# Kernel optimization log

Hardware: AMD Instinct MI355X
Metric: run time of the kernel (lower is better)

Reference implementation:

```python
import jax, jax.numpy as jnp
import numpy as np

H = 32  # hidden size


def _lstm_layer(x_sbi, w_ih, w_hh, b_ih, b_hh):
    # x_sbi: [S, B, in]; w_ih: [4H, in]; w_hh: [4H, H] (torch gate order i,f,g,o)
    S, B, _ = x_sbi.shape
    # precompute input projections for all timesteps: [S, B, 4H]
    xg = jnp.einsum('sbi,gi->sbg', x_sbi, w_ih) + (b_ih + b_hh)

    def step(carry, xg_t):
        h, c = carry
        gates = xg_t + h @ w_hh.T  # [B, 4H]
        i, f, g, o = jnp.split(gates, 4, axis=-1)
        i = jax.nn.sigmoid(i)
        f = jax.nn.sigmoid(f)
        g = jnp.tanh(g)
        o = jax.nn.sigmoid(o)
        c = f * c + i * g
        h = o * jnp.tanh(c)
        return (h, c), h

    h0 = jnp.zeros((B, H), x_sbi.dtype)
    c0 = jnp.zeros((B, H), x_sbi.dtype)
    (h_last, _), hs = jax.lax.scan(step, (h0, c0), xg)
    return hs, h_last  # hs: [S, B, H]


def setup_inputs() -> dict:
    key = jax.random.key(0)
    ks = jax.random.split(key, 12)
    B, S = 4096, 512
    s = 1.0 / np.sqrt(H)  # torch default uniform(-1/sqrt(H), 1/sqrt(H))
    u = lambda k, shape: jax.random.uniform(k, shape, jnp.float32, -s, s)
    return {
        'x': jax.random.normal(ks[0], (B, S, 1), jnp.float32),
        'w_ih0': u(ks[1], (4 * H, 1)),
        'w_hh0': u(ks[2], (4 * H, H)),
        'b_ih0': u(ks[3], (4 * H,)),
        'b_hh0': u(ks[4], (4 * H,)),
        'w_ih1': u(ks[5], (4 * H, H)),
        'w_hh1': u(ks[6], (4 * H, H)),
        'b_ih1': u(ks[7], (4 * H,)),
        'b_hh1': u(ks[8], (4 * H,)),
        'fc1_w': u(ks[9], (16, H)),
        'fc1_b': u(ks[9], (16,)),
        'fc2_w': u(ks[10], (1, 16)),
        'fc2_b': u(ks[11], (1,)),
    }


def reference(x, w_ih0, w_hh0, b_ih0, b_hh0, w_ih1, w_hh1, b_ih1, b_hh1,
              fc1_w, fc1_b, fc2_w, fc2_b):
    x_sbi = jnp.swapaxes(x, 0, 1)  # [S, B, 1]
    hs1, _ = _lstm_layer(x_sbi, w_ih0, w_hh0, b_ih0, b_hh0)
    _, h_last = _lstm_layer(hs1, w_ih1, w_hh1, b_ih1, b_hh1)  # last timestep of layer 2
    y = h_last @ fc1_w.T + fc1_b
    y = jnp.where(y >= 0, y, 0.2 * y)  # leaky_relu(0.2)
    y = y @ fc2_w.T + fc2_b
    return y  # [B, 1]
```

## Files before the change

kernel.cpp:

```cpp
#include <hip/hip_runtime.h>

#define H 32
#define SEQ 512
#define BM 16
#define NTHREADS 512
#define HSTRIDE 40

typedef _Float16 half8 __attribute__((ext_vector_type(8)));
typedef _Float16 f16x2 __attribute__((ext_vector_type(2)));
typedef __attribute__((ext_vector_type(4))) float f32x4;
typedef __attribute__((ext_vector_type(2))) float f32x2;

#define L2E 1.44269504088896340736f

__device__ __forceinline__ float rcp_(float x)  { return __builtin_amdgcn_rcpf(x); }
__device__ __forceinline__ float exp2_(float x) { return __builtin_amdgcn_exp2f(x); }
#define MFMA16(A, B, C) __builtin_amdgcn_mfma_f32_16x16x32_f16((A), (B), (C), 0, 0, 0)

__device__ __forceinline__ f32x2 cell2(const f32x4& ga, const f32x4& gb, f32x2& cst) {
    f32x2 ei = {exp2_(ga[0]), exp2_(gb[0])};
    f32x2 ef = {exp2_(ga[1]), exp2_(gb[1])};
    f32x2 eg = {exp2_(ga[2]), exp2_(gb[2])};
    f32x2 eo = {exp2_(ga[3]), exp2_(gb[3])};
    f32x2 A  = 1.f + ei, F = 1.f + ef;
    f32x2 Gp = eg + 1.f, Gm = eg - 1.f;
    f32x2 t1 = A * Gp;
    f32x2 num = __builtin_elementwise_fma(cst, t1, Gm * F);
    f32x2 den = F * t1;
    f32x2 r1 = {rcp_(den.x), rcp_(den.y)};
    f32x2 cn = num * r1;
    cst = cn;
    f32x2 arg = __builtin_elementwise_min(cn * (2.f * L2E), (f32x2)80.f);
    f32x2 ec = {exp2_(arg.x), exp2_(arg.y)};
    f32x2 dh = (1.f + eo) * (ec + 1.f);
    f32x2 r2 = {rcp_(dh.x), rcp_(dh.y)};
    return (ec - 1.f) * r2;
}

__global__ __launch_bounds__(NTHREADS, 2) void lstm_kernel(
    const float* __restrict__ x,
    const float* __restrict__ w_ih0,
    const float* __restrict__ w_hh0,
    const float* __restrict__ b_ih0, const float* __restrict__ b_hh0,
    const float* __restrict__ w_ih1,
    const float* __restrict__ w_hh1,
    const float* __restrict__ b_ih1, const float* __restrict__ b_hh1,
    const float* __restrict__ fc1_w,
    const float* __restrict__ fc1_b,
    const float* __restrict__ fc2_w,
    const float* __restrict__ fc2_b,
    float* __restrict__ out)
{
    __shared__ __align__(16) float    xbufT[(SEQ + 1) * BM];
    __shared__ __align__(16) _Float16 h1s[4][BM * HSTRIDE];
    __shared__ __align__(16) _Float16 h2s[2][BM * HSTRIDE];
    __shared__ __align__(16) float    h2f[BM * 33];
    __shared__ __align__(16) float    yb[BM * 17];

    const int tid  = threadIdx.x;
    const int lane = tid & 63;
    const int wv   = tid >> 6;
    const int role = wv >> 2;
    const int w    = wv & 3;
    const int c    = lane & 15;
    const int q    = lane >> 4;
    const int r0   = blockIdx.x * BM;

    {
        const int row = tid >> 5;
        const int s0  = (tid & 31) * 16;
        const float* xr = x + (size_t)(r0 + row) * SEQ + s0;
        #pragma unroll
        for (int i = 0; i < 16; i += 4) {
            float4 v = *(const float4*)&xr[i];
            xbufT[(s0 + i + 0) * BM + row] = v.x;
            xbufT[(s0 + i + 1) * BM + row] = v.y;
            xbufT[(s0 + i + 2) * BM + row] = v.z;
            xbufT[(s0 + i + 3) * BM + row] = v.w;
        }
    }
    for (int i = tid; i < 4 * BM * HSTRIDE; i += NTHREADS) ((_Float16*)h1s)[i] = (_Float16)0.f;
    for (int i = tid; i < 2 * BM * HSTRIDE; i += NTHREADS) ((_Float16*)h2s)[i] = (_Float16)0.f;

    const float gsc[4] = { -L2E, -L2E, 2.f * L2E, -L2E };
    const float wsc = gsc[c & 3];
    const int kb = 8 * q;
    const int m = c;

    half8 wA[2], wB[2];
    f32x4 biasv[2], wxv[2];
    #pragma unroll
    for (int k = 0; k < 2; ++k) {
        const int u     = 8 * w + 2 * q + k;
        const int worig = (c & 3) * H + 8 * w + 2 * (c >> 2) + k;
        if (role == 0) {
            const float* p = &w_hh0[worig * H + kb];
            #pragma unroll
            for (int j = 0; j < 8; ++j) wA[k][j] = (_Float16)(p[j] * wsc);
            #pragma unroll
            for (int g = 0; g < 4; ++g) {
                biasv[k][g] = (b_ih0[g * H + u] + b_hh0[g * H + u]) * gsc[g];
                wxv[k][g]   = w_ih0[g * H + u] * gsc[g];
            }
        } else {
            const float* p = &w_ih1[worig * H + kb];
            #pragma unroll
            for (int j = 0; j < 8; ++j) wA[k][j] = (_Float16)(p[j] * wsc);
            p = &w_hh1[worig * H + kb];
            #pragma unroll
            for (int j = 0; j < 8; ++j) wB[k][j] = (_Float16)(p[j] * wsc);
            #pragma unroll
            for (int g = 0; g < 4; ++g)
                biasv[k][g] = (b_ih1[g * H + u] + b_hh1[g * H + u]) * gsc[g];
        }
    }

    f32x2 cst = {0.f, 0.f};
    f32x2 hl  = {0.f, 0.f};

    const int fofs  = c * HSTRIDE + kb;
    const int whofs = m * HSTRIDE + 8 * w + 2 * q;

    f32x4 P[2][2] = {};

    __syncthreads();

    if (role == 0) __builtin_amdgcn_s_setprio(1);

    float xv = xbufT[m];

    for (int tb = 0; tb < 516; tb += 4) {
        #pragma unroll
        for (int p = 0; p < 4; ++p) {
            const int t = tb + p;
            if (role == 0) {
                if (t < 512) {
                    f32x4 pre[2];
                    #pragma unroll
                    for (int k = 0; k < 2; ++k) {
                        #pragma unroll
                        for (int j = 0; j < 4; ++j) pre[k][j] = fmaf(xv, wxv[k][j], biasv[k][j]);
                    }
                    half8 a1 = *(const half8*)(&h1s[(p + 3) & 3][0] + fofs);
                    f32x4 g0 = MFMA16(wA[0], a1, pre[0]);
                    f32x4 g1 = MFMA16(wA[1], a1, pre[1]);
                    f32x2 hv = cell2(g0, g1, cst);
                    f16x2 hp; hp[0] = (_Float16)hv.x; hp[1] = (_Float16)hv.y;
                    *(f16x2*)(&h1s[p][0] + whofs) = hp;
                    xv = xbufT[(t + 1) * BM + m];
                }
            } else {
                if (t >= 2 && t < 514) {
                    half8 a2 = *(const half8*)(&h2s[(p + 1) & 1][0] + fofs);
                    f32x4 g0 = MFMA16(wB[0], a2, P[p & 1][0]);
                    f32x4 g1 = MFMA16(wB[1], a2, P[p & 1][1]);
                    f32x2 hv = cell2(g0, g1, cst);
                    hl = hv;
                    f16x2 hp; hp[0] = (_Float16)hv.x; hp[1] = (_Float16)hv.y;
                    *(f16x2*)(&h2s[p & 1][0] + whofs) = hp;
                }
                if (t >= 1 && t < 513) {
                    half8 a1n = *(const half8*)(&h1s[(p + 3) & 3][0] + fofs);
                    P[(p + 1) & 1][0] = MFMA16(wA[0], a1n, biasv[0]);
                    P[(p + 1) & 1][1] = MFMA16(wA[1], a1n, biasv[1]);
                }
            }
            __syncthreads();
        }
    }

    if (role == 0) __builtin_amdgcn_s_setprio(0);

    if (role == 1) {
        h2f[m * 33 + (8 * w + 2 * q + 0)] = hl.x;
        h2f[m * 33 + (8 * w + 2 * q + 1)] = hl.y;
    }
    __syncthreads();
    if (tid < BM * 16) {
        int rr = tid >> 4, j = tid & 15;
        float acc = fc1_b[j];
        #pragma unroll
        for (int k = 0; k < H; ++k) acc += fc1_w[j * H + k] * h2f[rr * 33 + k];
        acc = acc >= 0.f ? acc : 0.2f * acc;
        yb[rr * 17 + j] = acc * fc2_w[j];
    }
    __syncthreads();
    if (tid < BM) {
        float acc = fc2_b[0];
        #pragma unroll
        for (int j = 0; j < 16; ++j) acc += yb[tid * 17 + j];
        out[r0 + tid] = acc;
    }
}

extern "C" void kernel_launch(void* const* d_in, const int* in_sizes, int n_in,
                              void* d_out, int out_size, void* d_ws, size_t ws_size,
                              hipStream_t stream) {
    const float* x     = (const float*)d_in[0];
    const float* w_ih0 = (const float*)d_in[1];
    const float* w_hh0 = (const float*)d_in[2];
    const float* b_ih0 = (const float*)d_in[3];
    const float* b_hh0 = (const float*)d_in[4];
    const float* w_ih1 = (const float*)d_in[5];
    const float* w_hh1 = (const float*)d_in[6];
    const float* b_ih1 = (const float*)d_in[7];
    const float* b_hh1 = (const float*)d_in[8];
    const float* fc1_w = (const float*)d_in[9];
    const float* fc1_b = (const float*)d_in[10];
    const float* fc2_w = (const float*)d_in[11];
    const float* fc2_b = (const float*)d_in[12];
    float* out = (float*)d_out;

    const int B = in_sizes[0] / SEQ;
    hipLaunchKernelGGL(lstm_kernel, dim3(B / BM), dim3(NTHREADS), 0, stream,
                       x, w_ih0, w_hh0, b_ih0, b_hh0, w_ih1, w_hh1, b_ih1, b_hh1,
                       fc1_w, fc1_b, fc2_w, fc2_b, out);
}
```

Baseline: 253.6 us.

## Halve batch tile to 8 rows with 4 waves, doubling MFMAs per wave

Shrinks each block from 16 batch rows and 8 waves to 8 rows and 4 waves. Each wave now covers 16 hidden units and issues four MFMAs per step, selecting results by lane half. This doubles the grid size and shrinks the barrier group, meant to improve CU fill and cut per-step sync latency. In exchange, half of the MFMA columns are duplicated work. It also adds an s_sleep stagger on the upper half of blocks.

New measurement: 275.4 us. +8.6%, slower.

```diff
diff --git a/kernel.cpp b/kernel.cpp
--- a/kernel.cpp
+++ b/kernel.cpp
@@ -2,8 +2,8 @@
 
 #define H 32
 #define SEQ 512
-#define BM 16
-#define NTHREADS 512
+#define BM 8
+#define NTHREADS 256
 #define HSTRIDE 40
 
 typedef _Float16 half8 __attribute__((ext_vector_type(8)));
@@ -60,23 +60,26 @@
     const int tid  = threadIdx.x;
     const int lane = tid & 63;
     const int wv   = tid >> 6;
-    const int role = wv >> 2;
-    const int w    = wv & 3;
+    const int role = wv >> 1;
+    const int wh   = wv & 1;
     const int c    = lane & 15;
     const int q    = lane >> 4;
+    const int row  = c & 7;
+    const int ch   = c >> 3;
+    const int U0   = 16 * wh;
     const int r0   = blockIdx.x * BM;
 
     {
-        const int row = tid >> 5;
-        const int s0  = (tid & 31) * 16;
-        const float* xr = x + (size_t)(r0 + row) * SEQ + s0;
+        const int xrow = tid >> 5;
+        const int s0   = (tid & 31) * 16;
+        const float* xr = x + (size_t)(r0 + xrow) * SEQ + s0;
         #pragma unroll
         for (int i = 0; i < 16; i += 4) {
             float4 v = *(const float4*)&xr[i];
-            xbufT[(s0 + i + 0) * BM + row] = v.x;
-            xbufT[(s0 + i + 1) * BM + row] = v.y;
-            xbufT[(s0 + i + 2) * BM + row] = v.z;
-            xbufT[(s0 + i + 3) * BM + row] = v.w;
+            xbufT[(s0 + i + 0) * BM + xrow] = v.x;
+            xbufT[(s0 + i + 1) * BM + xrow] = v.y;
+            xbufT[(s0 + i + 2) * BM + xrow] = v.z;
+            xbufT[(s0 + i + 3) * BM + xrow] = v.w;
         }
     }
     for (int i = tid; i < 4 * BM * HSTRIDE; i += NTHREADS) ((_Float16*)h1s)[i] = (_Float16)0.f;
@@ -85,49 +88,54 @@
     const float gsc[4] = { -L2E, -L2E, 2.f * L2E, -L2E };
     const float wsc = gsc[c & 3];
     const int kb = 8 * q;
-    const int m = c;
-
-    half8 wA[2], wB[2];
+
+    half8 wA[4], wB[4];
     f32x4 biasv[2], wxv[2];
     #pragma unroll
-    for (int k = 0; k < 2; ++k) {
-        const int u     = 8 * w + 2 * q + k;
-        const int worig = (c & 3) * H + 8 * w + 2 * (c >> 2) + k;
+    for (int kk = 0; kk < 4; ++kk) {
+        const int worig = (c & 3) * H + U0 + 8 * (kk >> 1) + 2 * (c >> 2) + (kk & 1);
         if (role == 0) {
             const float* p = &w_hh0[worig * H + kb];
             #pragma unroll
-            for (int j = 0; j < 8; ++j) wA[k][j] = (_Float16)(p[j] * wsc);
-            #pragma unroll
-            for (int g = 0; g < 4; ++g) {
-                biasv[k][g] = (b_ih0[g * H + u] + b_hh0[g * H + u]) * gsc[g];
-                wxv[k][g]   = w_ih0[g * H + u] * gsc[g];
-            }
+            for (int j = 0; j < 8; ++j) wA[kk][j] = (_Float16)(p[j] * wsc);
         } else {
             const float* p = &w_ih1[worig * H + kb];
             #pragma unroll
-            for (int j = 0; j < 8; ++j) wA[k][j] = (_Float16)(p[j] * wsc);
+            for (int j = 0; j < 8; ++j) wA[kk][j] = (_Float16)(p[j] * wsc);
             p = &w_hh1[worig * H + kb];
             #pragma unroll
-            for (int j = 0; j < 8; ++j) wB[k][j] = (_Float16)(p[j] * wsc);
-            #pragma unroll
-            for (int g = 0; g < 4; ++g)
+            for (int j = 0; j < 8; ++j) wB[kk][j] = (_Float16)(p[j] * wsc);
+        }
+    }
+    #pragma unroll
+    for (int k = 0; k < 2; ++k) {
+        const int u = U0 + 8 * ch + 2 * q + k;
+        #pragma unroll
+        for (int g = 0; g < 4; ++g) {
+            if (role == 0) {
+                biasv[k][g] = (b_ih0[g * H + u] + b_hh0[g * H + u]) * gsc[g];
+                wxv[k][g]   = w_ih0[g * H + u] * gsc[g];
+            } else {
                 biasv[k][g] = (b_ih1[g * H + u] + b_hh1[g * H + u]) * gsc[g];
+            }
         }
     }
 
     f32x2 cst = {0.f, 0.f};
     f32x2 hl  = {0.f, 0.f};
 
-    const int fofs  = c * HSTRIDE + kb;
-    const int whofs = m * HSTRIDE + 8 * w + 2 * q;
-
-    f32x4 P[2][2] = {};
+    const int fofs  = row * HSTRIDE + kb;
+    const int whofs = row * HSTRIDE + U0 + 8 * ch + 2 * q;
+
+    f32x4 P[2][4] = {};
 
     __syncthreads();
 
+    if (blockIdx.x & 256) __builtin_amdgcn_s_sleep(7);
+
     if (role == 0) __builtin_amdgcn_s_setprio(1);
 
-    float xv = xbufT[m];
+    float xv = xbufT[row];
 
     for (int tb = 0; tb < 516; tb += 4) {
         #pragma unroll
@@ -135,25 +143,37 @@
             const int t = tb + p;
             if (role == 0) {
                 if (t < 512) {
-                    f32x4 pre[2];
+                    f32x4 pre0, pre1;
                     #pragma unroll
-                    for (int k = 0; k < 2; ++k) {
-                        #pragma unroll
-                        for (int j = 0; j < 4; ++j) pre[k][j] = fmaf(xv, wxv[k][j], biasv[k][j]);
+                    for (int j = 0; j < 4; ++j) {
+                        pre0[j] = fmaf(xv, wxv[0][j], biasv[0][j]);
+                        pre1[j] = fmaf(xv, wxv[1][j], biasv[1][j]);
                     }
                     half8 a1 = *(const half8*)(&h1s[(p + 3) & 3][0] + fofs);
-                    f32x4 g0 = MFMA16(wA[0], a1, pre[0]);
-                    f32x4 g1 = MFMA16(wA[1], a1, pre[1]);
+                    f32x4 d0 = MFMA16(wA[0], a1, pre0);
+                    f32x4 d1 = MFMA16(wA[1], a1, pre1);
+                    f32x4 d2 = MFMA16(wA[2], a1, pre0);
+                    f32x4 d3 = MFMA16(wA[3], a1, pre1);
+                    f32x4 g0, g1;
+                    #pragma unroll
+                    for (int j = 0; j < 4; ++j) { g0[j] = ch ? d2[j] : d0[j];
+                                                  g1[j] = ch ? d3[j] : d1[j]; }
                     f32x2 hv = cell2(g0, g1, cst);
                     f16x2 hp; hp[0] = (_Float16)hv.x; hp[1] = (_Float16)hv.y;
                     *(f16x2*)(&h1s[p][0] + whofs) = hp;
-                    xv = xbufT[(t + 1) * BM + m];
+                    xv = xbufT[(t + 1) * BM + row];
                 }
             } else {
                 if (t >= 2 && t < 514) {
                     half8 a2 = *(const half8*)(&h2s[(p + 1) & 1][0] + fofs);
-                    f32x4 g0 = MFMA16(wB[0], a2, P[p & 1][0]);
-                    f32x4 g1 = MFMA16(wB[1], a2, P[p & 1][1]);
+                    f32x4 d0 = MFMA16(wB[0], a2, P[p & 1][0]);
+                    f32x4 d1 = MFMA16(wB[1], a2, P[p & 1][1]);
+                    f32x4 d2 = MFMA16(wB[2], a2, P[p & 1][2]);
+                    f32x4 d3 = MFMA16(wB[3], a2, P[p & 1][3]);
+                    f32x4 g0, g1;
+                    #pragma unroll
+                    for (int j = 0; j < 4; ++j) { g0[j] = ch ? d2[j] : d0[j];
+                                                  g1[j] = ch ? d3[j] : d1[j]; }
                     f32x2 hv = cell2(g0, g1, cst);
                     hl = hv;
                     f16x2 hp; hp[0] = (_Float16)hv.x; hp[1] = (_Float16)hv.y;
@@ -163,6 +183,8 @@
                     half8 a1n = *(const half8*)(&h1s[(p + 3) & 3][0] + fofs);
                     P[(p + 1) & 1][0] = MFMA16(wA[0], a1n, biasv[0]);
                     P[(p + 1) & 1][1] = MFMA16(wA[1], a1n, biasv[1]);
+                    P[(p + 1) & 1][2] = MFMA16(wA[2], a1n, biasv[0]);
+                    P[(p + 1) & 1][3] = MFMA16(wA[3], a1n, biasv[1]);
                 }
             }
             __syncthreads();
@@ -172,8 +194,8 @@
     if (role == 0) __builtin_amdgcn_s_setprio(0);
 
     if (role == 1) {
-        h2f[m * 33 + (8 * w + 2 * q + 0)] = hl.x;
-        h2f[m * 33 + (8 * w + 2 * q + 1)] = hl.y;
+        h2f[row * 33 + (U0 + 8 * ch + 2 * q + 0)] = hl.x;
+        h2f[row * 33 + (U0 + 8 * ch + 2 * q + 1)] = hl.y;
     }
     __syncthreads();
     if (tid < BM * 16) {
```

## Make each wave own four batch rows for both layers and drop block barriers

Applied to the files above, without the earlier changes.

Work is split by batch row instead of by layer. Each 64-lane wave computes layer 1, layer 2 and the layer-2 input projection for its own four rows across all 32 hidden units. Because each wave only reads hidden state it wrote itself, the per-timestep __syncthreads is removed and the block shrinks to 256 threads. In exchange each wave issues 8 MFMAs per matrix product and keeps only a quarter of the outputs, selected per lane, which raises MFMA work about fourfold. Each wave also holds all three weight matrices in registers, and layer-1 and layer-2 cells now run serially in one wave rather than on separate waves.

Measured after the change: 383.9 us. 1.51x slower.

```diff
diff --git a/kernel.cpp b/kernel.cpp
--- a/kernel.cpp
+++ b/kernel.cpp
@@ -3,7 +3,7 @@
 #define H 32
 #define SEQ 512
 #define BM 16
-#define NTHREADS 512
+#define NTHREADS 256
 #define HSTRIDE 40
 
 typedef _Float16 half8 __attribute__((ext_vector_type(8)));
@@ -37,7 +37,20 @@
     return (ec - 1.f) * r2;
 }
 
-__global__ __launch_bounds__(NTHREADS, 2) void lstm_kernel(
+__device__ __forceinline__ f32x4 sel4(const f32x4& a0, const f32x4& a1,
+                                      const f32x4& a2, const f32x4& a3,
+                                      bool s0, bool s1) {
+    f32x4 r;
+    #pragma unroll
+    for (int j = 0; j < 4; ++j) {
+        float t0 = s0 ? a1[j] : a0[j];
+        float t1 = s0 ? a3[j] : a2[j];
+        r[j] = s1 ? t1 : t0;
+    }
+    return r;
+}
+
+__global__ __launch_bounds__(NTHREADS, 1) void lstm_kernel(
     const float* __restrict__ x,
     const float* __restrict__ w_ih0,
     const float* __restrict__ w_hh0,
@@ -52,7 +65,7 @@
     float* __restrict__ out)
 {
     __shared__ __align__(16) float    xbufT[(SEQ + 1) * BM];
-    __shared__ __align__(16) _Float16 h1s[4][BM * HSTRIDE];
+    __shared__ __align__(16) _Float16 h1s[2][BM * HSTRIDE];
     __shared__ __align__(16) _Float16 h2s[2][BM * HSTRIDE];
     __shared__ __align__(16) float    h2f[BM * 33];
     __shared__ __align__(16) float    yb[BM * 17];
@@ -60,123 +73,123 @@
     const int tid  = threadIdx.x;
     const int lane = tid & 63;
     const int wv   = tid >> 6;
-    const int role = wv >> 2;
-    const int w    = wv & 3;
     const int c    = lane & 15;
     const int q    = lane >> 4;
+    const int s    = c >> 2;
+    const bool sb0 = s & 1, sb1 = (s >> 1) & 1;
+    const int row  = 4 * wv + (c & 3);
     const int r0   = blockIdx.x * BM;
 
     {
-        const int row = tid >> 5;
-        const int s0  = (tid & 31) * 16;
-        const float* xr = x + (size_t)(r0 + row) * SEQ + s0;
-        #pragma unroll
-        for (int i = 0; i < 16; i += 4) {
+        const int xrow = tid >> 4;
+        const int s0_  = (tid & 15) * 32;
+        const float* xr = x + (size_t)(r0 + xrow) * SEQ + s0_;
+        #pragma unroll
+        for (int i = 0; i < 32; i += 4) {
             float4 v = *(const float4*)&xr[i];
-            xbufT[(s0 + i + 0) * BM + row] = v.x;
-            xbufT[(s0 + i + 1) * BM + row] = v.y;
-            xbufT[(s0 + i + 2) * BM + row] = v.z;
-            xbufT[(s0 + i + 3) * BM + row] = v.w;
-        }
-    }
-    for (int i = tid; i < 4 * BM * HSTRIDE; i += NTHREADS) ((_Float16*)h1s)[i] = (_Float16)0.f;
-    for (int i = tid; i < 2 * BM * HSTRIDE; i += NTHREADS) ((_Float16*)h2s)[i] = (_Float16)0.f;
+            xbufT[(s0_ + i + 0) * BM + xrow] = v.x;
+            xbufT[(s0_ + i + 1) * BM + xrow] = v.y;
+            xbufT[(s0_ + i + 2) * BM + xrow] = v.z;
+            xbufT[(s0_ + i + 3) * BM + xrow] = v.w;
+        }
+    }
+    for (int i = tid; i < 2 * BM * HSTRIDE; i += NTHREADS) {
+        ((_Float16*)h1s)[i] = (_Float16)0.f;
+        ((_Float16*)h2s)[i] = (_Float16)0.f;
+    }
 
     const float gsc[4] = { -L2E, -L2E, 2.f * L2E, -L2E };
     const float wsc = gsc[c & 3];
     const int kb = 8 * q;
-    const int m = c;
-
-    half8 wA[2], wB[2];
-    f32x4 biasv[2], wxv[2];
+
+    half8 wA0[8], wI1[8], wH1[8];
+    #pragma unroll
+    for (int kk = 0; kk < 8; ++kk) {
+        const int worig = (c & 3) * H + 8 * (kk >> 1) + 2 * (c >> 2) + (kk & 1);
+        const float* p = &w_hh0[worig * H + kb];
+        #pragma unroll
+        for (int j = 0; j < 8; ++j) wA0[kk][j] = (_Float16)(p[j] * wsc);
+        p = &w_ih1[worig * H + kb];
+        #pragma unroll
+        for (int j = 0; j < 8; ++j) wI1[kk][j] = (_Float16)(p[j] * wsc);
+        p = &w_hh1[worig * H + kb];
+        #pragma unroll
+        for (int j = 0; j < 8; ++j) wH1[kk][j] = (_Float16)(p[j] * wsc);
+    }
+    f32x4 b1v[2], wxv[2], b2v[2];
     #pragma unroll
     for (int k = 0; k < 2; ++k) {
-        const int u     = 8 * w + 2 * q + k;
-        const int worig = (c & 3) * H + 8 * w + 2 * (c >> 2) + k;
-        if (role == 0) {
-            const float* p = &w_hh0[worig * H + kb];
-            #pragma unroll
-            for (int j = 0; j < 8; ++j) wA[k][j] = (_Float16)(p[j] * wsc);
-            #pragma unroll
-            for (int g = 0; g < 4; ++g) {
-                biasv[k][g] = (b_ih0[g * H + u] + b_hh0[g * H + u]) * gsc[g];
-                wxv[k][g]   = w_ih0[g * H + u] * gsc[g];
+        const int u = 8 * s + 2 * q + k;
+        #pragma unroll
+        for (int g = 0; g < 4; ++g) {
+            b1v[k][g] = (b_ih0[g * H + u] + b_hh0[g * H + u]) * gsc[g];
+            wxv[k][g] = w_ih0[g * H + u] * gsc[g];
+            b2v[k][g] = (b_ih1[g * H + u] + b_hh1[g * H + u]) * gsc[g];
+        }
+    }
+
+    f32x2 cst1 = {0.f, 0.f}, cst2 = {0.f, 0.f};
+    f32x2 hl = {0.f, 0.f};
+    f32x4 Pf[8] = {};
+
+    const int fofs  = row * HSTRIDE + kb;
+    const int whofs = row * HSTRIDE + 8 * s + 2 * q;
+
+    __syncthreads();
+
+    float xv = xbufT[row];
+
+    auto step = [&](int t, int P, bool doL1, bool doL2, bool doP) {
+        half8 B1 = *(const half8*)(&h1s[P ^ 1][0] + fofs);
+        half8 B2 = *(const half8*)(&h2s[P ^ 1][0] + fofs);
+        if (doL2) {
+            f32x4 a[8];
+            #pragma unroll
+            for (int kk = 0; kk < 8; ++kk) a[kk] = MFMA16(wH1[kk], B2, Pf[kk]);
+            f32x4 ga = sel4(a[0], a[2], a[4], a[6], sb0, sb1);
+            f32x4 gb = sel4(a[1], a[3], a[5], a[7], sb0, sb1);
+            f32x2 hv = cell2(ga, gb, cst2);
+            hl = hv;
+            f16x2 hp; hp[0] = (_Float16)hv.x; hp[1] = (_Float16)hv.y;
+            *(f16x2*)(&h2s[P][0] + whofs) = hp;
+        }
+        if (doL1) {
+            f32x4 pre0, pre1;
+            #pragma unroll
+            for (int j = 0; j < 4; ++j) {
+                pre0[j] = fmaf(xv, wxv[0][j], b1v[0][j]);
+                pre1[j] = fmaf(xv, wxv[1][j], b1v[1][j]);
             }
-        } else {
-            const float* p = &w_ih1[worig * H + kb];
-            #pragma unroll
-            for (int j = 0; j < 8; ++j) wA[k][j] = (_Float16)(p[j] * wsc);
-            p = &w_hh1[worig * H + kb];
-            #pragma unroll
-            for (int j = 0; j < 8; ++j) wB[k][j] = (_Float16)(p[j] * wsc);
-            #pragma unroll
-            for (int g = 0; g < 4; ++g)
-                biasv[k][g] = (b_ih1[g * H + u] + b_hh1[g * H + u]) * gsc[g];
-        }
-    }
-
-    f32x2 cst = {0.f, 0.f};
-    f32x2 hl  = {0.f, 0.f};
-
-    const int fofs  = c * HSTRIDE + kb;
-    const int whofs = m * HSTRIDE + 8 * w + 2 * q;
-
-    f32x4 P[2][2] = {};
-
+            f32x4 a[8];
+            #pragma unroll
+            for (int kk = 0; kk < 8; ++kk) a[kk] = MFMA16(wA0[kk], B1, (kk & 1) ? pre1 : pre0);
+            f32x4 ga = sel4(a[0], a[2], a[4], a[6], sb0, sb1);
+            f32x4 gb = sel4(a[1], a[3], a[5], a[7], sb0, sb1);
+            f32x2 hv = cell2(ga, gb, cst1);
+            f16x2 hp; hp[0] = (_Float16)hv.x; hp[1] = (_Float16)hv.y;
+            *(f16x2*)(&h1s[P][0] + whofs) = hp;
+            xv = xbufT[(t + 1) * BM + row];
+        }
+        if (doP) {
+            #pragma unroll
+            for (int kk = 0; kk < 8; ++kk)
+                Pf[kk] = MFMA16(wI1[kk], B1, (kk & 1) ? b2v[1] : b2v[0]);
+        }
+    };
+
+    step(0, 0, true, false, false);
+    step(1, 1, true, false, true);
+    for (int tb = 2; tb < 512; tb += 2) {
+        step(tb,     0, true, true, true);
+        step(tb + 1, 1, true, true, true);
+    }
+    step(512, 0, false, true, true);
+    step(513, 1, false, true, false);
+
+    h2f[row * 33 + (8 * s + 2 * q + 0)] = hl.x;
+    h2f[row * 33 + (8 * s + 2 * q + 1)] = hl.y;
     __syncthreads();
-
-    if (role == 0) __builtin_amdgcn_s_setprio(1);
-
-    float xv = xbufT[m];
-
-    for (int tb = 0; tb < 516; tb += 4) {
-        #pragma unroll
-        for (int p = 0; p < 4; ++p) {
-            const int t = tb + p;
-            if (role == 0) {
-                if (t < 512) {
-                    f32x4 pre[2];
-                    #pragma unroll
-                    for (int k = 0; k < 2; ++k) {
-                        #pragma unroll
-                        for (int j = 0; j < 4; ++j) pre[k][j] = fmaf(xv, wxv[k][j], biasv[k][j]);
-                    }
-                    half8 a1 = *(const half8*)(&h1s[(p + 3) & 3][0] + fofs);
-                    f32x4 g0 = MFMA16(wA[0], a1, pre[0]);
-                    f32x4 g1 = MFMA16(wA[1], a1, pre[1]);
-                    f32x2 hv = cell2(g0, g1, cst);
-                    f16x2 hp; hp[0] = (_Float16)hv.x; hp[1] = (_Float16)hv.y;
-                    *(f16x2*)(&h1s[p][0] + whofs) = hp;
-                    xv = xbufT[(t + 1) * BM + m];
-                }
-            } else {
-                if (t >= 2 && t < 514) {
-                    half8 a2 = *(const half8*)(&h2s[(p + 1) & 1][0] + fofs);
-                    f32x4 g0 = MFMA16(wB[0], a2, P[p & 1][0]);
-                    f32x4 g1 = MFMA16(wB[1], a2, P[p & 1][1]);
-                    f32x2 hv = cell2(g0, g1, cst);
-                    hl = hv;
-                    f16x2 hp; hp[0] = (_Float16)hv.x; hp[1] = (_Float16)hv.y;
-                    *(f16x2*)(&h2s[p & 1][0] + whofs) = hp;
-                }
-                if (t >= 1 && t < 513) {
-                    half8 a1n = *(const half8*)(&h1s[(p + 3) & 3][0] + fofs);
-                    P[(p + 1) & 1][0] = MFMA16(wA[0], a1n, biasv[0]);
-                    P[(p + 1) & 1][1] = MFMA16(wA[1], a1n, biasv[1]);
-                }
-            }
-            __syncthreads();
-        }
-    }
-
-    if (role == 0) __builtin_amdgcn_s_setprio(0);
-
-    if (role == 1) {
-        h2f[m * 33 + (8 * w + 2 * q + 0)] = hl.x;
-        h2f[m * 33 + (8 * w + 2 * q + 1)] = hl.y;
-    }
-    __syncthreads();
-    if (tid < BM * 16) {
+    {
         int rr = tid >> 4, j = tid & 15;
         float acc = fc1_b[j];
         #pragma unroll
```
